# Kernel tuning notes

Hardware: AMD Instinct MI355X
Metric: run time of the kernel (lower is better)

## Reference

```python
import jax, jax.numpy as jnp
import numpy as np

N, E, Z, C, B, G, T = 10000, 160000, 10, 64, 8, 16, 2
R_MAX = 5.0
AVG_NEIGH = 16.0
L_SLICES = ((0, 1), (1, 4), (4, 9))  # l=0,1,2 blocks of the 9 SH components


def sph_harm(u):
    # component-normalized real spherical harmonics up to l=2, u: [E,3] unit vectors
    x, y, z = u[:, 0], u[:, 1], u[:, 2]
    s3, s5, s15 = 3.0 ** 0.5, 5.0 ** 0.5, 15.0 ** 0.5
    return jnp.stack([
        jnp.ones_like(x),
        s3 * x, s3 * y, s3 * z,
        s15 * x * y, s15 * y * z, (s5 / 2) * (3 * z * z - 1), s15 * x * z, (s15 / 2) * (x * x - y * y),
    ], axis=1)  # [E,9]


def radial_embed(r):
    # Bessel basis * polynomial cutoff (p=5), r: [E]
    u = r / R_MAX
    n = jnp.arange(1, B + 1, dtype=jnp.float32)
    bessel = jnp.sqrt(2.0 / R_MAX) * jnp.sin(n[None, :] * jnp.pi * u[:, None]) / (r[:, None] + 1e-9)
    p = 5.0
    fc = 1 - (p + 1) * (p + 2) / 2 * u ** p + p * (p + 2) * u ** (p + 1) - p * (p + 1) / 2 * u ** (p + 2)
    fc = jnp.where(u < 1.0, fc, 0.0)
    return bessel * fc[:, None]  # [E,B]


def per_l_linear(x, W):
    # x: [n,C,9], W: [3,C,C]; independent channel mixing per l-block
    return jnp.concatenate([
        jnp.einsum('ncm,cd->ndm', x[:, :, s:e], W[l]) for l, (s, e) in enumerate(L_SLICES)
    ], axis=2)


def _forward(positions, node_attrs, charges, shifts, W_emb, atomic_energies,
             W_r1, W_r2, W_mix, W_sc, w_poly, W_prod, w_e, w_d,
             edge_index, batch, num_graphs):
    sender, receiver = edge_index[0], edge_index[1]
    # atomic reference energies
    node_e0 = node_attrs @ atomic_energies  # [N]
    e0 = jax.ops.segment_sum(node_e0, batch, num_segments=num_graphs)
    # node embedding: scalars only
    node_feats = jnp.zeros((positions.shape[0], C, 9), positions.dtype)
    node_feats = node_feats.at[:, :, 0].set(node_attrs @ W_emb)
    # edge geometry
    vec = positions[sender] - positions[receiver] + shifts  # [E,3]
    lengths = jnp.sqrt(jnp.sum(vec * vec, axis=1) + 1e-12)
    sh = sph_harm(vec / lengths[:, None])        # [E,9]
    edge_feats = radial_embed(lengths)           # [E,B]
    energies = [e0]
    dipoles = []
    for t in range(T):
        # radial MLP -> per-channel TP weights
        w = jax.nn.silu(edge_feats @ W_r1[t]) @ W_r2[t]      # [E,C]
        h_s = node_feats[sender, :, 0]                       # gather sender scalars [E,C]
        m = (w * h_s)[:, :, None] * sh[:, None, :]           # TP message [E,C,9]
        agg = jax.ops.segment_sum(m, receiver, num_segments=positions.shape[0]) / AVG_NEIGH
        msg = per_l_linear(agg, W_mix[t])
        sc = per_l_linear(node_feats, W_sc[t])               # self-connection
        # product basis (correlation 3): channel-wise scalar polynomial gate
        s0 = msg[:, :, 0]
        poly = w_poly[t, :, 0][None] + w_poly[t, :, 1][None] * s0 + w_poly[t, :, 2][None] * s0 * s0
        node_feats = per_l_linear(msg * poly[:, :, None], W_prod[t]) + sc
        # readout: 1x0e energy + 1x1o dipole
        e_n = node_feats[:, :, 0] @ w_e[t]                   # [N]
        energies.append(jax.ops.segment_sum(e_n, batch, num_segments=num_graphs))
        dipoles.append(jnp.einsum('ncm,c->nm', node_feats[:, :, 1:4], w_d[t]))  # [N,3]
    contributions = jnp.stack(energies, axis=-1)             # [G,T+1]
    total_energy = jnp.sum(contributions, axis=-1)           # [G]
    atomic_dipoles = jnp.sum(jnp.stack(dipoles, axis=-1), axis=-1)  # [N,3]
    total_dipole = jax.ops.segment_sum(atomic_dipoles, batch, num_segments=num_graphs)
    total_dipole = total_dipole + jax.ops.segment_sum(charges[:, None] * positions, batch, num_segments=num_graphs)
    return total_energy, contributions, atomic_dipoles, total_dipole


def setup_inputs():
    key = jax.random.key(0)
    ks = jax.random.split(key, 16)
    s = 0.1
    species = jax.random.randint(ks[1], (N,), 0, Z)
    return {
        'positions': jax.random.normal(ks[0], (N, 3)) * 3.0,
        'node_attrs': jax.nn.one_hot(species, Z, dtype=jnp.float32),
        'charges': jax.random.normal(ks[2], (N,)) * 0.1,
        'shifts': jnp.zeros((E, 3), jnp.float32),
        'W_emb': jax.random.normal(ks[5], (Z, C)) * s,
        'atomic_energies': jax.random.normal(ks[6], (Z,)) * s,
        'W_r1': jax.random.normal(ks[7], (T, B, 64)) * s,
        'W_r2': jax.random.normal(ks[8], (T, 64, C)) * s,
        'W_mix': jax.random.normal(ks[9], (T, 3, C, C)) * s,
        'W_sc': jax.random.normal(ks[10], (T, 3, C, C)) * s,
        'w_poly': jax.random.normal(ks[11], (T, C, 3)) * s,
        'W_prod': jax.random.normal(ks[12], (T, 3, C, C)) * s,
        'w_e': jax.random.normal(ks[13], (T, C)) * s,
        'w_d': jax.random.normal(ks[14], (T, C)) * s,
        'edge_index': jax.random.randint(ks[3], (2, E), 0, N),
        'batch': jnp.sort(jax.random.randint(ks[4], (N,), 0, G)),
        'num_graphs': G,
    }


def reference(positions, node_attrs, charges, shifts, W_emb, atomic_energies,
              W_r1, W_r2, W_mix, W_sc, w_poly, W_prod, w_e, w_d,
              edge_index, batch, num_graphs):
    args = (node_attrs, charges, shifts, W_emb, atomic_energies, W_r1, W_r2,
            W_mix, W_sc, w_poly, W_prod, w_e, w_d, edge_index, batch, num_graphs)
    total_energy, contributions, atomic_dipoles, total_dipole = _forward(positions, *args)
    forces = -jax.grad(lambda p: jnp.sum(_forward(p, *args)[0]))(positions)
    return total_energy, contributions, forces, total_dipole, atomic_dipoles
```

## Files before the change

### kernel.cpp

```cpp
#include <hip/hip_runtime.h>
#include <hip/hip_bf16.h>

#define NN 10000
#define NE 160000
#define NZ 10
#define NBES 8
#define NG 16
#define NT 2
#define NB 2048
#define NB1 2049
#define PL ((size_t)NN*64)

static constexpr float PI_F  = 3.14159265358979323846f;
static constexpr float KBES  = 0.63245553203367587f;
static constexpr float S3    = 1.73205080756887729f;

static constexpr size_t OFF_UVL  = 0;
static constexpr size_t OFF_PIN  = OFF_UVL + (size_t)NE*4;
static constexpr size_t OFF_ATT  = OFF_PIN + (size_t)NN*3;
static constexpr size_t OFF_CHG  = OFF_ATT + (size_t)NN*NZ;
static constexpr size_t OFF_SHF  = OFF_CHG + (size_t)NN;
static constexpr size_t OFF_NF0  = OFF_SHF + (size_t)NE*3;
static constexpr size_t OFF_NF1  = OFF_NF0 + PL;
static constexpr size_t OFF_MSG0 = OFF_NF1 + 4*PL;
static constexpr size_t OFF_MSG1 = OFF_MSG0 + 4*PL;
static constexpr size_t OFF_AGG  = OFF_MSG1 + 4*PL;
static constexpr size_t O_GA1    = OFF_MSG0 + PL;
static constexpr size_t O_GA0    = OFF_AGG;
static constexpr size_t OFF_W    = OFF_AGG + 4*PL;
static constexpr size_t O_WEMB   = OFF_W;
static constexpr size_t O_AE     = O_WEMB + 640;
static constexpr size_t O_R1     = O_AE   + 16;
static constexpr size_t O_R2     = O_R1   + 1024;
static constexpr size_t O_WMIX   = O_R2   + 8192;
static constexpr size_t O_WMIXT  = O_WMIX + 24576;
static constexpr size_t O_WSC    = O_WMIXT+ 24576;
static constexpr size_t O_WSCT   = O_WSC  + 24576;
static constexpr size_t O_WPROD  = O_WSCT + 24576;
static constexpr size_t O_WPRODT = O_WPROD+ 24576;
static constexpr size_t O_WPOLY  = O_WPRODT+24576;
static constexpr size_t O_WE     = O_WPOLY+ 384;
static constexpr size_t O_WD     = O_WE   + 128;
static constexpr size_t OFF_ACC  = O_WD   + 128;
static constexpr size_t O_E0G    = OFF_ACC;
static constexpr size_t O_ETG    = O_E0G + 16;
static constexpr size_t O_TD     = O_ETG + 32;
static constexpr size_t O_ADP    = O_TD  + 48;
static constexpr size_t O_GPOS   = O_ADP + (size_t)NN*3;
static constexpr size_t ACC_FLOATS = 96 + (size_t)NN*6;
static constexpr size_t O_EN0    = O_GPOS + (size_t)NN*3;
static constexpr size_t O_EN1    = O_EN0 + NN;
static constexpr size_t O_E0N    = O_EN1 + NN;
static constexpr size_t O_FLAG   = O_E0N + NN;
static constexpr size_t O_TW     = O_FLAG + 4;
static constexpr size_t O_TQ     = O_TW + (size_t)2*NB1*128;
static constexpr size_t O_OFFR   = O_TQ + (size_t)2*NB1*128;
static constexpr size_t O_OFFS   = O_OFFR + (NN+1);
static constexpr size_t O_CURR   = O_OFFS + (NN+1);
static constexpr size_t O_CURS   = O_CURR + NN;
static constexpr size_t O_RECRAW = O_CURS + NN;
static constexpr size_t O_RECR   = (O_RECRAW + 7) & ~(size_t)7;
static constexpr size_t O_RECS   = O_RECR + (size_t)NE*8 + 64;
static constexpr size_t WS_FLOATS= O_RECS + (size_t)NE*8 + 64;

__device__ __forceinline__ float rlane(float v, int l){
  return __int_as_float(__builtin_amdgcn_readlane(__float_as_int(v), l));
}
__device__ __forceinline__ int irlane(float v, int l){
  return __builtin_amdgcn_readlane(__float_as_int(v), l);
}

static constexpr int LD_CNT[14] = {NN*3, NN*NZ, NN, NE*3, NZ*64, NZ, NT*NBES*64, NT*64*64,
                                   NT*3*64*64, NT*3*64*64, NT*64*3, NT*3*64*64, NT*64, NT*64};
static constexpr int LD_TOTAL = NN*3 + NN*NZ + NN + NE*3 + NZ*64 + NZ + NT*NBES*64 + NT*64*64
                              + 3*(NT*3*64*64) + NT*64*3 + 4*(NT*64) - NT*64*2;
__global__ __launch_bounds__(256) void k_load_all(
    const void* s0, const void* s1, const void* s2, const void* s3, const void* s4,
    const void* s5, const void* s6, const void* s7, const void* s8, const void* s9,
    const void* s10, const void* s11, const void* s12, const void* s13,
    float* __restrict__ ws){
  __shared__ int found;
  if (threadIdx.x == 0) found = 0;
  __syncthreads();
  const unsigned* raw = (const unsigned*)s1;
  int f = 0;
  for (int i = threadIdx.x; i < 4096; i += 256){
    unsigned w = raw[i];
    f |= (w == 0x00003F80u || w == 0x3F803F80u) ? 1 : 0;
  }
  if (f) found = 1;
  __syncthreads();
  const int isbf = found;
  if (blockIdx.x == 0 && threadIdx.x == 0) ((int*)(ws + O_FLAG))[0] = isbf;

  const void* srcs[14] = {s0,s1,s2,s3,s4,s5,s6,s7,s8,s9,s10,s11,s12,s13};
  const size_t dsts[14] = {OFF_PIN, OFF_ATT, OFF_CHG, OFF_SHF, O_WEMB, O_AE, O_R1, O_R2,
                           O_WMIX, O_WSC, O_WPOLY, O_WPROD, O_WE, O_WD};
  int i = blockIdx.x*256 + threadIdx.x;
  int seg = -1, off = i;
  #pragma unroll
  for (int j = 0; j < 14; ++j){
    if (seg < 0){
      if (off < LD_CNT[j]) seg = j;
      else off -= LD_CNT[j];
    }
  }
  if (seg < 0) return;
  float v = isbf ? __bfloat162float(((const __hip_bfloat16*)srcs[seg])[off])
                 : ((const float*)srcs[seg])[off];
  ws[dsts[seg] + off] = v;
}

static constexpr int GEOM_B = (NE+255)/256;
static constexpr int TAB_B  = (2*NB1+3)/4;
static constexpr int INIT_B = (NN+3)/4;
static constexpr int TRAN_B = 5*4096/256;
__global__ __launch_bounds__(256, 3) void k_prep(float* __restrict__ ws, const int* __restrict__ ei){
  int b = blockIdx.x;
  if (b < GEOM_B){
    int e = b*256 + threadIdx.x;
    if (e >= NE) return;
    const float* pos = ws + OFF_PIN;
    const float* shifts = ws + OFF_SHF;
    int s = ei[e], r = ei[NE + e];
    float vx = pos[s*3+0] - pos[r*3+0] + shifts[(size_t)e*3+0];
    float vy = pos[s*3+1] - pos[r*3+1] + shifts[(size_t)e*3+1];
    float vz = pos[s*3+2] - pos[r*3+2] + shifts[(size_t)e*3+2];
    float L = sqrtf(vx*vx + vy*vy + vz*vz + 1e-12f);
    float inv = 1.f / L;
    float4 uq; uq.x = vx*inv; uq.y = vy*inv; uq.z = vz*inv; uq.w = L;
    *(float4*)(ws + OFF_UVL + (size_t)e*4) = uq;
    if (L < 5.f){
      atomicAdd((int*)(ws + O_CURR) + r, 1);
      atomicAdd((int*)(ws + O_CURS) + s, 1);
    }
  } else if (b < GEOM_B + TAB_B){
    int lane = threadIdx.x & 63;
    int task = (b - GEOM_B)*4 + (threadIdx.x >> 6);
    if (task >= 2*NB1) return;
    int t = task / NB1, node = task % NB1;
    const float* R1 = ws + O_R1 + (size_t)t*512;
    const float* R2 = ws + O_R2 + (size_t)t*4096;
    float r1c[8];
    #pragma unroll
    for (int j = 0; j < 8; ++j) r1c[j] = R1[j*64 + lane];
    float L = fmaxf((float)node * (5.f/NB), 1e-6f);
    float ur = L*0.2f;
    float ef[8], dd[8];
    if (ur < 1.f){
      float u2=ur*ur, u4=u2*u2, u5=u4*ur;
      float fc = 1.f - 21.f*u5 + 35.f*u5*ur - 15.f*u5*u2;
      float omu = 1.f - ur;
      float dfc = -105.f*u4*omu*omu;
      float invr = 1.f/(L + 1e-9f);
      #pragma unroll
      for (int bb = 0; bb < 8; ++bb){
        float nb = (float)(bb+1);
        float arg = nb*PI_F*ur;
        float sn = __sinf(arg), cs = __cosf(arg);
        float bes = KBES*sn*invr;
        float dbes = KBES*(nb*PI_F*0.2f)*cs*invr - bes*invr;
        ef[bb] = bes*fc;
        dd[bb] = dbes*fc + bes*dfc*0.2f;
      }
    } else {
      #pragma unroll
      for (int bb = 0; bb < 8; ++bb){ ef[bb] = 0.f; dd[bb] = 0.f; }
    }
    float a = 0.f, tt = 0.f;
    #pragma unroll
    for (int bb = 0; bb < 8; ++bb){ a = fmaf(ef[bb], r1c[bb], a); tt = fmaf(r1c[bb], dd[bb], tt); }
    float sg = 1.f/(1.f + __expf(-a));
    float sl = a*sg;
    float q  = sg*fmaf(a, 1.f - sg, 1.f)*tt;
    float r2c[64];
    #pragma unroll
    for (int j = 0; j < 64; ++j) r2c[j] = R2[j*64 + lane];
    float W0=0.f, W1=0.f, Q0=0.f, Q1=0.f;
    #pragma unroll
    for (int j = 0; j < 64; j += 2){
      W0 = fmaf(rlane(sl, j  ), r2c[j  ], W0);
      W1 = fmaf(rlane(sl, j+1), r2c[j+1], W1);
      Q0 = fmaf(rlane(q,  j  ), r2c[j  ], Q0);
      Q1 = fmaf(rlane(q,  j+1), r2c[j+1], Q1);
    }
    float Wv = (W0+W1)*(1.f/16.f);
    float Qv = (Q0+Q1)*(1.f/16.f);
    size_t base2 = ((size_t)t*NB1 + node)*128 + (size_t)lane*2;
    ws[O_TW + base2] = Wv;
    ws[O_TQ + base2] = Qv;
    if (node > 0){
      ws[O_TW + base2 - 128 + 1] = Wv;
      ws[O_TQ + base2 - 128 + 1] = Qv;
    }
  } else if (b < GEOM_B + TAB_B + INIT_B){
    int lane = threadIdx.x & 63;
    int n = (b - GEOM_B - TAB_B)*4 + (threadIdx.x >> 6);
    if (n >= NN) return;
    const float* attrs = ws + OFF_ATT;
    float acc = 0.f;
    #pragma unroll
    for (int z = 0; z < NZ; ++z) acc = fmaf(attrs[(size_t)n*NZ+z], ws[O_WEMB + z*64 + lane], acc);
    ws[OFF_NF0 + (size_t)n*64 + lane] = acc;
    if (lane == 0){
      float e = 0.f;
      #pragma unroll
      for (int z = 0; z < NZ; ++z) e = fmaf(attrs[(size_t)n*NZ+z], ws[O_AE + z], e);
      ws[O_E0N + n] = e;
    }
  } else {
    int i = (b - GEOM_B - TAB_B - INIT_B)*256 + threadIdx.x;
    int mat = i >> 12, r = (i >> 6) & 63, c = i & 63;
    const size_t src[5] = {O_WMIX, O_WMIX+12288, O_WPROD, O_WPROD+12288, O_WSC+12288};
    const size_t dst[5] = {O_WMIXT, O_WMIXT+12288, O_WPRODT, O_WPRODT+12288, O_WSCT+12288};
    ws[dst[mat] + (size_t)c*64 + r] = ws[src[mat] + (size_t)r*64 + c];
  }
}

__global__ __launch_bounds__(1024) void k_csr_scan(
    int* __restrict__ curr, int* __restrict__ curs,
    int* __restrict__ offr, int* __restrict__ offs_){
  __shared__ unsigned short cr[NN], cs[NN];
  __shared__ int pr[1024], ps[1024];
  int tid = threadIdx.x;
  for (int i = tid; i < NN; i += 1024){
    cr[i] = (unsigned short)curr[i];
    cs[i] = (unsigned short)curs[i];
  }
  __syncthreads();
  const int chunk = (NN + 1023)/1024;
  int lo = tid*chunk, hi = lo + chunk;
  if (hi > NN) hi = NN;
  if (lo > NN) lo = NN;
  int sr = 0, ss = 0;
  for (int i = lo; i < hi; ++i){ sr += cr[i]; ss += cs[i]; }
  pr[tid] = sr; ps[tid] = ss;
  __syncthreads();
  for (int o = 1; o < 1024; o <<= 1){
    int vr = (tid >= o) ? pr[tid-o] : 0;
    int vs = (tid >= o) ? ps[tid-o] : 0;
    __syncthreads();
    pr[tid] += vr; ps[tid] += vs;
    __syncthreads();
  }
  int runr = tid ? pr[tid-1] : 0;
  int runs = tid ? ps[tid-1] : 0;
  for (int i = lo; i < hi; ++i){
    int a = cr[i], c = cs[i];
    offr[i] = runr; curr[i] = runr; runr += a;
    offs_[i] = runs; curs[i] = runs; runs += c;
  }
  if (tid == 1023){ offr[NN] = runr; offs_[NN] = runs; }
}

__global__ void k_csr_fill(const int* __restrict__ ei, const float* __restrict__ uvl,
                           int* __restrict__ curr, int* __restrict__ curs,
                           float* __restrict__ recr, float* __restrict__ recs){
  int e = blockIdx.x*256 + threadIdx.x;
  if (e >= NE) return;
  float4 q = *(const float4*)(uvl + (size_t)e*4);
  if (q.w >= 5.f) return;
  int s = ei[e], r = ei[NE + e];
  int4 meta; meta.x = s; meta.y = r; meta.z = e; meta.w = 0;
  int pr = atomicAdd(&curr[r], 1);
  *(float4*)(recr + (size_t)pr*8) = q;
  *(int4*)(recr + (size_t)pr*8 + 4) = meta;
  int ps = atomicAdd(&curs[s], 1);
  *(float4*)(recs + (size_t)ps*8) = q;
  *(int4*)(recs + (size_t)ps*8 + 4) = meta;
}

__global__ __launch_bounds__(256, 4) void k_agg(
    const float* __restrict__ TWt, const float* __restrict__ recr,
    const float* __restrict__ h, const int* __restrict__ offr,
    float* __restrict__ agg){
  int lane = threadIdx.x & 63;
  int wid = blockIdx.x*4 + (threadIdx.x >> 6);
  int nw  = gridDim.x*4;
  for (int n = wid; n < NN; n += nw){
    int lo = offr[n], hi = offr[n+1];
    float c0=0.f, x1=0.f, y1=0.f, z1=0.f;
    if (lo < hi){
      float rv = recr[(size_t)lo*8 + lane];
      for (int i = lo; i < hi; ){
        int ni = i + 8;
        float rvn = (ni < hi) ? recr[(size_t)ni*8 + lane] : 0.f;
        int cnt = hi - i;
        if (cnt >= 8){
          #pragma unroll
          for (int j = 0; j < 8; ++j){
            float ux = rlane(rv, j*8+0), uy = rlane(rv, j*8+1), uz = rlane(rv, j*8+2);
            float L  = rlane(rv, j*8+3);
            int   s  = irlane(rv, j*8+4);
            float pos = L*(NB/5.f); int bi = (int)pos; float f = pos - (float)bi;
            const float2 tp = *(const float2*)(TWt + ((size_t)bi*64 + lane)*2);
            float w = fmaf(tp.y - tp.x, f, tp.x);
            float wh = w * h[(size_t)s*64 + lane];
            c0 += wh;
            x1 = fmaf(wh, ux, x1);
            y1 = fmaf(wh, uy, y1);
            z1 = fmaf(wh, uz, z1);
          }
        } else {
          for (int j = 0; j < cnt; ++j){
            float ux = rlane(rv, j*8+0), uy = rlane(rv, j*8+1), uz = rlane(rv, j*8+2);
            float L  = rlane(rv, j*8+3);
            int   s  = irlane(rv, j*8+4);
            float pos = L*(NB/5.f); int bi = (int)pos; float f = pos - (float)bi;
            const float2 tp = *(const float2*)(TWt + ((size_t)bi*64 + lane)*2);
            float w = fmaf(tp.y - tp.x, f, tp.x);
            float wh = w * h[(size_t)s*64 + lane];
            c0 += wh;
            x1 = fmaf(wh, ux, x1);
            y1 = fmaf(wh, uy, y1);
            z1 = fmaf(wh, uz, z1);
          }
        }
        rv = rvn; i = ni;
      }
    }
    size_t ob = (size_t)n*64 + lane;
    agg[ob]        = c0;
    agg[ob+PL]     = S3*x1;
    agg[ob+2*PL]   = S3*y1;
    agg[ob+3*PL]   = S3*z1;
  }
}

template<int GB1>
__global__ __launch_bounds__(256, 3) void k_lin2(
    const float* __restrict__ in, const float* __restrict__ W3, float* __restrict__ out,
    const float* __restrict__ WMIXT1, const float* __restrict__ WPRODT1,
    const float* __restrict__ we1, const float* __restrict__ wp1,
    float* __restrict__ ga1){
  int k = blockIdx.y;
  int l = (k==0) ? 0 : 1;
  const float* W = W3 + (size_t)l*4096;
  int lane = threadIdx.x & 63;
  float wcol[64];
  #pragma unroll
  for (int j = 0; j < 64; ++j) wcol[j] = W[j*64 + lane];
  float wcol2[64];
  float g = 0.f, p0 = 0.f, p1 = 0.f, p2 = 0.f;
  const bool gb1 = GB1 && (k == 0);
  if (gb1){
    #pragma unroll
    for (int j = 0; j < 64; ++j) wcol2[j] = WMIXT1[j*64 + lane];
    #pragma unroll
    for (int c = 0; c < 64; ++c) g = fmaf(we1[c], WPRODT1[c*64 + lane], g);
    p0 = wp1[lane*3]; p1 = wp1[lane*3+1]; p2 = wp1[lane*3+2];
  }
  int wid = blockIdx.x*4 + (threadIdx.x >> 6);
  int nw  = gridDim.x*4;
  const float* inp = in + (size_t)k*PL;
  float* outp = out + (size_t)k*PL;
  for (int n = wid; n < NN; n += nw){
    float x = inp[(size_t)n*64 + lane];
    float a0 = 0.f, a1 = 0.f, a2 = 0.f, a3 = 0.f;
    #pragma unroll
    for (int j = 0; j < 64; j += 4){
      a0 = fmaf(rlane(x, j  ), wcol[j  ], a0);
      a1 = fmaf(rlane(x, j+1), wcol[j+1], a1);
      a2 = fmaf(rlane(x, j+2), wcol[j+2], a2);
      a3 = fmaf(rlane(x, j+3), wcol[j+3], a3);
    }
    float m = (a0+a1) + (a2+a3);
    outp[(size_t)n*64 + lane] = m;
    if (gb1){
      float poly = fmaf(fmaf(p2, m, p1), m, p0);
      float dp   = fmaf(2.f*p2, m, p1);
      float gb = g*fmaf(m, dp, poly);
      float b0=0.f, b1=0.f, b2=0.f, b3=0.f;
      #pragma unroll
      for (int j = 0; j < 64; j += 4){
        b0 = fmaf(rlane(gb, j  ), wcol2[j  ], b0);
        b1 = fmaf(rlane(gb, j+1), wcol2[j+1], b1);
        b2 = fmaf(rlane(gb, j+2), wcol2[j+2], b2);
        b3 = fmaf(rlane(gb, j+3), wcol2[j+3], b3);
      }
      ga1[(size_t)n*64 + lane] = (b0+b1) + (b2+b3);
    }
  }
}

template<int WRITE_NF, int NF_SINGLE>
__global__ __launch_bounds__(256, 3) void k_tail(
    const float* __restrict__ nf_in, const float* __restrict__ msg,
    const float* __restrict__ Wsc, const float* __restrict__ Wprod, const float* __restrict__ wp,
    const float* __restrict__ we, const float* __restrict__ wd,
    float* __restrict__ nf_out, float* __restrict__ en, float* __restrict__ adp){
  int lane = threadIdx.x & 63;
  int k = threadIdx.x >> 6;
  int l = (k==0) ? 0 : 1;
  const bool use_sc = !(NF_SINGLE && k > 0);
  float wcs[64], wcp[64];
  #pragma unroll
  for (int j = 0; j < 64; ++j)
    wcp[j] = Wprod[(size_t)l*4096 + j*64 + lane];
  if (use_sc){
    #pragma unroll
    for (int j = 0; j < 64; ++j)
      wcs[j] = Wsc[(size_t)l*4096 + j*64 + lane];
  }
  float p0 = wp[lane*3], p1 = wp[lane*3+1], p2 = wp[lane*3+2];
  float rw = (k==0) ? we[lane] : wd[lane];
  const float* msgk = msg + (size_t)k*PL;
  const float* nfk  = nf_in + (size_t)k*PL;
  float* outk = nf_out + (size_t)k*PL;
  for (int n = blockIdx.x; n < NN; n += gridDim.x){
    size_t base = (size_t)n*64 + lane;
    float s0 = msg[base];
    float xm = (k==0) ? s0 : msgk[base];
    float xg = xm * fmaf(fmaf(p2, s0, p1), s0, p0);
    float b0=0.f, b1=0.f;
    #pragma unroll
    for (int j = 0; j < 64; j += 2){
      b0 = fmaf(rlane(xg, j  ), wcp[j  ], b0);
      b1 = fmaf(rlane(xg, j+1), wcp[j+1], b1);
    }
    float out = b0 + b1;
    if (use_sc){
      float xs = nfk[base];
      float a0=0.f, a1=0.f;
      #pragma unroll
      for (int j = 0; j < 64; j += 2){
        a0 = fmaf(rlane(xs, j  ), wcs[j  ], a0);
        a1 = fmaf(rlane(xs, j+1), wcs[j+1], a1);
      }
      out += a0 + a1;
    }
    if (WRITE_NF) outk[base] = out;
    float red = out * rw;
    #pragma unroll
    for (int o = 32; o; o >>= 1) red += __shfl_xor(red, o, 64);
    if (lane == 0){
      if (k == 0) en[n] = red;
      else        adp[n*3 + (k-1)] += red;
    }
  }
}

static constexpr int GHG_GRID = 1024;
static constexpr int RED_B = (NN+255)/256;
__global__ __launch_bounds__(256, 2) void k_ghg0(float* __restrict__ ws, const int* __restrict__ offs_,
                                                 const int* __restrict__ batch){
  if (blockIdx.x >= GHG_GRID){
    int n = (blockIdx.x - GHG_GRID)*256 + threadIdx.x;
    int lane = threadIdx.x & 63;
    bool valid = (n < NN);
    int g = valid ? batch[n] : -1;
    float v0=0.f, v1=0.f, v2=0.f, tx=0.f, ty=0.f, tz=0.f;
    if (valid){
      v0 = ws[O_E0N + n]; v1 = ws[O_EN0 + n]; v2 = ws[O_EN1 + n];
      float qq = ws[OFF_CHG + n];
      tx = ws[O_ADP + n*3+0] + qq*ws[OFF_PIN + n*3+0];
      ty = ws[O_ADP + n*3+1] + qq*ws[OFF_PIN + n*3+1];
      tz = ws[O_ADP + n*3+2] + qq*ws[OFF_PIN + n*3+2];
    }
    float* e0g = ws + O_E0G; float* Etg = ws + O_ETG; float* td = ws + O_TD;
    int g0 = __shfl(g, 0, 64), g63 = __shfl(g, 63, 64);
    if (g0 == g63 && g0 >= 0){
      #pragma unroll
      for (int o = 32; o; o >>= 1){
        v0 += __shfl_xor(v0, o, 64); v1 += __shfl_xor(v1, o, 64); v2 += __shfl_xor(v2, o, 64);
        tx += __shfl_xor(tx, o, 64); ty += __shfl_xor(ty, o, 64); tz += __shfl_xor(tz, o, 64);
      }
      if (lane == 0){
        atomicAdd(&e0g[g0], v0); atomicAdd(&Etg[g0], v1); atomicAdd(&Etg[16+g0], v2);
        atomicAdd(&td[g0*3+0], tx); atomicAdd(&td[g0*3+1], ty); atomicAdd(&td[g0*3+2], tz);
      }
    } else if (valid){
      atomicAdd(&e0g[g], v0); atomicAdd(&Etg[g], v1); atomicAdd(&Etg[16+g], v2);
      atomicAdd(&td[g*3+0], tx); atomicAdd(&td[g*3+1], ty); atomicAdd(&td[g*3+2], tz);
    }
    return;
  }
  const int lane = threadIdx.x & 63;
  float wcp[64], wcm[64];
  #pragma unroll
  for (int j = 0; j < 64; ++j) wcp[j] = ws[O_WPRODT + j*64 + lane];
  #pragma unroll
  for (int j = 0; j < 64; ++j) wcm[j] = ws[O_WMIXT + j*64 + lane];
  int wid = blockIdx.x*4 + (threadIdx.x >> 6);
  const int nw = GHG_GRID*4;
  float gnfc = ws[O_WE + lane];
  {
    const float* WS1 = ws + O_WSCT + 12288;
    const float* we1 = ws + O_WE + 64;
    #pragma unroll
    for (int c = 0; c < 64; ++c) gnfc = fmaf(we1[c], WS1[c*64 + lane], gnfc);
  }
  const float p0 = ws[O_WPOLY + lane*3];
  const float p1 = ws[O_WPOLY + lane*3 + 1];
  const float p2 = ws[O_WPOLY + lane*3 + 2];
  const float* TW1 = ws + O_TW + (size_t)NB1*128;
  const float* recs = ws + O_RECS;
  const float* GA1 = ws + O_GA1;
  for (int n = wid; n < NN; n += nw){
    int lo = offs_[n], hi = offs_[n+1];
    float acc = 0.f;
    if (lo < hi){
      float rv = recs[(size_t)lo*8 + lane];
      for (int i = lo; i < hi; ){
        int ni = i + 8;
        float rvn = (ni < hi) ? recs[(size_t)ni*8 + lane] : 0.f;
        int cnt = hi - i;
        if (cnt >= 8){
          #pragma unroll
          for (int j = 0; j < 8; ++j){
            float L = rlane(rv, j*8+3);
            int   r = irlane(rv, j*8+5);
            float pos = L*(NB/5.f); int bi = (int)pos; float f = pos - (float)bi;
            const float2 tp = *(const float2*)(TW1 + ((size_t)bi*64 + lane)*2);
            float w = fmaf(tp.y - tp.x, f, tp.x);
            acc = fmaf(w, GA1[(size_t)r*64 + lane], acc);
          }
        } else {
          for (int j = 0; j < cnt; ++j){
            float L = rlane(rv, j*8+3);
            int   r = irlane(rv, j*8+5);
            float pos = L*(NB/5.f); int bi = (int)pos; float f = pos - (float)bi;
            const float2 tp = *(const float2*)(TW1 + ((size_t)bi*64 + lane)*2);
            float w = fmaf(tp.y - tp.x, f, tp.x);
            acc = fmaf(w, GA1[(size_t)r*64 + lane], acc);
          }
        }
        rv = rvn; i = ni;
      }
    }
    float gB = gnfc + acc;
    float q0=0.f, q1=0.f;
    #pragma unroll
    for (int j = 0; j < 64; j += 2){
      q0 = fmaf(rlane(gB,j),   wcp[j  ], q0);
      q1 = fmaf(rlane(gB,j+1), wcp[j+1], q1);
    }
    float gmp = q0 + q1;
    float s0v = ws[OFF_MSG0 + (size_t)n*64 + lane];
    float poly = fmaf(fmaf(p2, s0v, p1), s0v, p0);
    float dp   = fmaf(2.f*p2, s0v, p1);
    float gb = gmp * fmaf(s0v, dp, poly);
    float u0=0.f, u1=0.f;
    #pragma unroll
    for (int j = 0; j < 64; j += 2){
      u0 = fmaf(rlane(gb,j),   wcm[j  ], u0);
      u1 = fmaf(rlane(gb,j+1), wcm[j+1], u1);
    }
    ws[O_GA0 + (size_t)n*64 + lane] = u0 + u1;
  }
}

__global__ __launch_bounds__(256, 4) void k_bwdE2(float* __restrict__ ws, const int* __restrict__ nlive_ptr){
  const int lane = threadIdx.x & 63;
  int wid = blockIdx.x*4 + (threadIdx.x >> 6);
  const int nw = gridDim.x*4;
  const int nlive = nlive_ptr[0];
  const int ngrp = (nlive + 7) >> 3;
  const float* recs = ws + O_RECS;
  const float* TQ0 = ws + O_TQ;
  const float* TQ1 = ws + O_TQ + (size_t)NB1*128;
  const float* h0  = ws + OFF_NF0;
  const float* h1  = ws + OFF_NF1;
  const float* ga0 = ws + O_GA0;
  const float* ga1 = ws + O_GA1;
  float* gpos = ws + O_GPOS;
  for (int gi = wid; gi < ngrp; gi += nw){
    const int i0 = gi*8;
    float rv = recs[(size_t)i0*8 + lane];
    int cnt = nlive - i0; if (cnt > 8) cnt = 8;
    #pragma unroll 8
    for (int j = 0; j < cnt; ++j){
      float ux = rlane(rv, j*8+0), uy = rlane(rv, j*8+1), uz = rlane(rv, j*8+2);
      float L  = rlane(rv, j*8+3);
      int   s  = irlane(rv, j*8+4);
      int   r  = irlane(rv, j*8+5);
      float pos = L*(NB/5.f); int bi = (int)pos; float f = pos - (float)bi;
      const float2 t0 = *(const float2*)(TQ0 + ((size_t)bi*64 + lane)*2);
      const float2 t1 = *(const float2*)(TQ1 + ((size_t)bi*64 + lane)*2);
      float Q0 = fmaf(t0.y - t0.x, f, t0.x);
      float Q1 = fmaf(t1.y - t1.x, f, t1.x);
      float rr = Q0*h0[(size_t)s*64 + lane]*ga0[(size_t)r*64 + lane]
               + Q1*h1[(size_t)s*64 + lane]*ga1[(size_t)r*64 + lane];
      #pragma unroll
      for (int o = 32; o; o >>= 1) rr += __shfl_xor(rr, o, 64);
      if (lane < 3){
        float u = (lane==0) ? ux : ((lane==1) ? uy : uz);
        float v = rr*u;
        atomicAdd(&gpos[(size_t)s*3 + lane],  v);
        atomicAdd(&gpos[(size_t)r*3 + lane], -v);
      }
    }
  }
}

__global__ void k_writeout(const float* __restrict__ e0g, const float* __restrict__ Etg,
                           const float* __restrict__ td, const float* __restrict__ adp,
                           const float* __restrict__ gpos, void* __restrict__ outv,
                           const int* __restrict__ flag){
  int i = blockIdx.x*256 + threadIdx.x;
  const int total = NG + NG*3 + NN*3 + NG*3 + NN*3;
  if (i >= total) return;
  float v;
  if (i < 16){
    v = e0g[i] + Etg[i] + Etg[16+i];
  } else if (i < 64){
    int j = i - 16; int g = j/3, t = j - g*3;
    v = (t == 0) ? e0g[g] : Etg[(t-1)*16 + g];
  } else if (i < 64 + NN*3){
    v = -gpos[i-64];
  } else if (i < 64 + NN*3 + 48){
    v = td[i - (64 + NN*3)];
  } else {
    v = adp[i - (64 + NN*3 + 48)];
  }
  if (flag[0]) ((__hip_bfloat16*)outv)[i] = __float2bfloat16(v);
  else         ((float*)outv)[i] = v;
}

extern "C" void kernel_launch(void* const* d_in, const int* in_sizes, int n_in,
                              void* d_out, int out_size, void* d_ws, size_t ws_size,
                              hipStream_t stream) {
  if (ws_size < WS_FLOATS*sizeof(float)) return;
  const int* ei    = (const int*)d_in[14];
  const int* batch = (const int*)d_in[15];
  float* ws = (float*)d_ws;

  int* offr  = (int*)(ws + O_OFFR);
  int* offs_ = (int*)(ws + O_OFFS);
  int* curr  = (int*)(ws + O_CURR);
  int* curs  = (int*)(ws + O_CURS);

  hipMemsetAsync(ws + OFF_ACC, 0, ACC_FLOATS*sizeof(float), stream);
  hipMemsetAsync(curr, 0, 2*NN*sizeof(int), stream);

  k_load_all<<<(LD_TOTAL+255)/256, 256, 0, stream>>>(
      d_in[0], d_in[1], d_in[2], d_in[3], d_in[4], d_in[5], d_in[6], d_in[7],
      d_in[8], d_in[9], d_in[10], d_in[11], d_in[12], d_in[13], ws);
  k_prep<<<GEOM_B + TAB_B + INIT_B + TRAN_B, 256, 0, stream>>>(ws, ei);
  k_csr_scan<<<1, 1024, 0, stream>>>(curr, curs, offr, offs_);
  k_csr_fill<<<(NE+255)/256, 256, 0, stream>>>(ei, ws+OFF_UVL, curr, curs,
                                               ws+O_RECR, ws+O_RECS);

  dim3 ling(256, 4);

  k_agg<<<1024, 256, 0, stream>>>(ws+O_TW, ws+O_RECR, ws+OFF_NF0, offr, ws+OFF_AGG);
  k_lin2<0><<<ling, 256, 0, stream>>>(ws+OFF_AGG, ws+O_WMIX, ws+OFF_MSG0,
                                      ws, ws, ws, ws, ws);
  k_tail<1,1><<<1024, 256, 0, stream>>>(ws+OFF_NF0, ws+OFF_MSG0,
                                        ws+O_WSC, ws+O_WPROD,
                                        ws+O_WPOLY, ws+O_WE, ws+O_WD,
                                        ws+OFF_NF1, ws+O_EN0, ws+O_ADP);
  k_agg<<<1024, 256, 0, stream>>>(ws+O_TW + (size_t)NB1*128, ws+O_RECR, ws+OFF_NF1, offr, ws+OFF_AGG);
  k_lin2<1><<<ling, 256, 0, stream>>>(ws+OFF_AGG, ws+O_WMIX + 12288, ws+OFF_MSG1,
                                      ws+O_WMIXT + 12288, ws+O_WPRODT + 12288,
                                      ws+O_WE + 64, ws+O_WPOLY + 192, ws+O_GA1);
  k_tail<0,0><<<1024, 256, 0, stream>>>(ws+OFF_NF1, ws+OFF_MSG1,
                                        ws+O_WSC + 12288, ws+O_WPROD + 12288,
                                        ws+O_WPOLY + 192, ws+O_WE + 64, ws+O_WD + 64,
                                        ws+OFF_NF1, ws+O_EN1, ws+O_ADP);

  k_ghg0<<<GHG_GRID + RED_B, 256, 0, stream>>>(ws, offs_, batch);
  k_bwdE2<<<2048, 256, 0, stream>>>(ws, offs_ + NN);

  k_writeout<<<(60112+255)/256, 256, 0, stream>>>(ws+O_E0G, ws+O_ETG, ws+O_TD, ws+O_ADP,
                                                  ws+O_GPOS, d_out, (const int*)(ws+O_FLAG));
}
```

Before: 335.0 us.

## Replace CSR construction with compacted edge list and atomic scatter aggregation

After: 387.7 us. 1.16x slower.

```diff
diff --git a/kernel.cpp b/kernel.cpp
--- a/kernel.cpp
+++ b/kernel.cpp
@@ -27,6 +27,7 @@
 static constexpr size_t OFF_AGG  = OFF_MSG1 + 4*PL;
 static constexpr size_t O_GA1    = OFF_MSG0 + PL;
 static constexpr size_t O_GA0    = OFF_AGG;
+static constexpr size_t O_GB0    = OFF_AGG + PL;
 static constexpr size_t OFF_W    = OFF_AGG + 4*PL;
 static constexpr size_t O_WEMB   = OFF_W;
 static constexpr size_t O_AE     = O_WEMB + 640;
@@ -54,13 +55,8 @@
 static constexpr size_t O_FLAG   = O_E0N + NN;
 static constexpr size_t O_TW     = O_FLAG + 4;
 static constexpr size_t O_TQ     = O_TW + (size_t)2*NB1*128;
-static constexpr size_t O_OFFR   = O_TQ + (size_t)2*NB1*128;
-static constexpr size_t O_OFFS   = O_OFFR + (NN+1);
-static constexpr size_t O_CURR   = O_OFFS + (NN+1);
-static constexpr size_t O_CURS   = O_CURR + NN;
-static constexpr size_t O_RECRAW = O_CURS + NN;
-static constexpr size_t O_RECR   = (O_RECRAW + 7) & ~(size_t)7;
-static constexpr size_t O_RECS   = O_RECR + (size_t)NE*8 + 64;
+static constexpr size_t O_RECRAW = O_TQ + (size_t)2*NB1*128;
+static constexpr size_t O_RECS   = (O_RECRAW + 7) & ~(size_t)7;
 static constexpr size_t WS_FLOATS= O_RECS + (size_t)NE*8 + 64;
 
 __device__ __forceinline__ float rlane(float v, int l){
@@ -127,12 +123,14 @@
     float vy = pos[s*3+1] - pos[r*3+1] + shifts[(size_t)e*3+1];
     float vz = pos[s*3+2] - pos[r*3+2] + shifts[(size_t)e*3+2];
     float L = sqrtf(vx*vx + vy*vy + vz*vz + 1e-12f);
-    float inv = 1.f / L;
-    float4 uq; uq.x = vx*inv; uq.y = vy*inv; uq.z = vz*inv; uq.w = L;
-    *(float4*)(ws + OFF_UVL + (size_t)e*4) = uq;
     if (L < 5.f){
-      atomicAdd((int*)(ws + O_CURR) + r, 1);
-      atomicAdd((int*)(ws + O_CURS) + s, 1);
+      int p = atomicAdd((int*)(ws + O_FLAG) + 1, 1);
+      float inv = 1.f / L;
+      float* rec = ws + O_RECS + (size_t)p*8;
+      float4 uq; uq.x = vx*inv; uq.y = vy*inv; uq.z = vz*inv; uq.w = L;
+      *(float4*)rec = uq;
+      int4 meta; meta.x = s; meta.y = r; meta.z = e; meta.w = 0;
+      *(int4*)(rec + 4) = meta;
     }
   } else if (b < GEOM_B + TAB_B){
     int lane = threadIdx.x & 63;
@@ -217,119 +215,41 @@
   }
 }
 
-__global__ __launch_bounds__(1024) void k_csr_scan(
-    int* __restrict__ curr, int* __restrict__ curs,
-    int* __restrict__ offr, int* __restrict__ offs_){
-  __shared__ unsigned short cr[NN], cs[NN];
-  __shared__ int pr[1024], ps[1024];
-  int tid = threadIdx.x;
-  for (int i = tid; i < NN; i += 1024){
-    cr[i] = (unsigned short)curr[i];
-    cs[i] = (unsigned short)curs[i];
-  }
-  __syncthreads();
-  const int chunk = (NN + 1023)/1024;
-  int lo = tid*chunk, hi = lo + chunk;
-  if (hi > NN) hi = NN;
-  if (lo > NN) lo = NN;
-  int sr = 0, ss = 0;
-  for (int i = lo; i < hi; ++i){ sr += cr[i]; ss += cs[i]; }
-  pr[tid] = sr; ps[tid] = ss;
-  __syncthreads();
-  for (int o = 1; o < 1024; o <<= 1){
-    int vr = (tid >= o) ? pr[tid-o] : 0;
-    int vs = (tid >= o) ? ps[tid-o] : 0;
-    __syncthreads();
-    pr[tid] += vr; ps[tid] += vs;
-    __syncthreads();
-  }
-  int runr = tid ? pr[tid-1] : 0;
-  int runs = tid ? ps[tid-1] : 0;
-  for (int i = lo; i < hi; ++i){
-    int a = cr[i], c = cs[i];
-    offr[i] = runr; curr[i] = runr; runr += a;
-    offs_[i] = runs; curs[i] = runs; runs += c;
-  }
-  if (tid == 1023){ offr[NN] = runr; offs_[NN] = runs; }
-}
-
-__global__ void k_csr_fill(const int* __restrict__ ei, const float* __restrict__ uvl,
-                           int* __restrict__ curr, int* __restrict__ curs,
-                           float* __restrict__ recr, float* __restrict__ recs){
-  int e = blockIdx.x*256 + threadIdx.x;
-  if (e >= NE) return;
-  float4 q = *(const float4*)(uvl + (size_t)e*4);
-  if (q.w >= 5.f) return;
-  int s = ei[e], r = ei[NE + e];
-  int4 meta; meta.x = s; meta.y = r; meta.z = e; meta.w = 0;
-  int pr = atomicAdd(&curr[r], 1);
-  *(float4*)(recr + (size_t)pr*8) = q;
-  *(int4*)(recr + (size_t)pr*8 + 4) = meta;
-  int ps = atomicAdd(&curs[s], 1);
-  *(float4*)(recs + (size_t)ps*8) = q;
-  *(int4*)(recs + (size_t)ps*8 + 4) = meta;
-}
-
-__global__ __launch_bounds__(256, 4) void k_agg(
-    const float* __restrict__ TWt, const float* __restrict__ recr,
-    const float* __restrict__ h, const int* __restrict__ offr,
+__global__ __launch_bounds__(256, 4) void k_aggE(
+    const float* __restrict__ TWt, const float* __restrict__ recs,
+    const int* __restrict__ nlive_ptr, const float* __restrict__ h,
     float* __restrict__ agg){
-  int lane = threadIdx.x & 63;
+  const int lane = threadIdx.x & 63;
   int wid = blockIdx.x*4 + (threadIdx.x >> 6);
-  int nw  = gridDim.x*4;
-  for (int n = wid; n < NN; n += nw){
-    int lo = offr[n], hi = offr[n+1];
-    float c0=0.f, x1=0.f, y1=0.f, z1=0.f;
-    if (lo < hi){
-      float rv = recr[(size_t)lo*8 + lane];
-      for (int i = lo; i < hi; ){
-        int ni = i + 8;
-        float rvn = (ni < hi) ? recr[(size_t)ni*8 + lane] : 0.f;
-        int cnt = hi - i;
-        if (cnt >= 8){
-          #pragma unroll
-          for (int j = 0; j < 8; ++j){
-            float ux = rlane(rv, j*8+0), uy = rlane(rv, j*8+1), uz = rlane(rv, j*8+2);
-            float L  = rlane(rv, j*8+3);
-            int   s  = irlane(rv, j*8+4);
-            float pos = L*(NB/5.f); int bi = (int)pos; float f = pos - (float)bi;
-            const float2 tp = *(const float2*)(TWt + ((size_t)bi*64 + lane)*2);
-            float w = fmaf(tp.y - tp.x, f, tp.x);
-            float wh = w * h[(size_t)s*64 + lane];
-            c0 += wh;
-            x1 = fmaf(wh, ux, x1);
-            y1 = fmaf(wh, uy, y1);
-            z1 = fmaf(wh, uz, z1);
-          }
-        } else {
-          for (int j = 0; j < cnt; ++j){
-            float ux = rlane(rv, j*8+0), uy = rlane(rv, j*8+1), uz = rlane(rv, j*8+2);
-            float L  = rlane(rv, j*8+3);
-            int   s  = irlane(rv, j*8+4);
-            float pos = L*(NB/5.f); int bi = (int)pos; float f = pos - (float)bi;
-            const float2 tp = *(const float2*)(TWt + ((size_t)bi*64 + lane)*2);
-            float w = fmaf(tp.y - tp.x, f, tp.x);
-            float wh = w * h[(size_t)s*64 + lane];
-            c0 += wh;
-            x1 = fmaf(wh, ux, x1);
-            y1 = fmaf(wh, uy, y1);
-            z1 = fmaf(wh, uz, z1);
-          }
-        }
-        rv = rvn; i = ni;
-      }
-    }
-    size_t ob = (size_t)n*64 + lane;
-    agg[ob]        = c0;
-    agg[ob+PL]     = S3*x1;
-    agg[ob+2*PL]   = S3*y1;
-    agg[ob+3*PL]   = S3*z1;
+  const int nw = gridDim.x*4;
+  const int nlive = nlive_ptr[0];
+  const int ngrp = (nlive + 7) >> 3;
+  for (int gi = wid; gi < ngrp; gi += nw){
+    const int i0 = gi*8;
+    float rv = recs[(size_t)i0*8 + lane];
+    int cnt = nlive - i0; if (cnt > 8) cnt = 8;
+    #pragma unroll 8
+    for (int j = 0; j < cnt; ++j){
+      float ux = rlane(rv, j*8+0), uy = rlane(rv, j*8+1), uz = rlane(rv, j*8+2);
+      float L  = rlane(rv, j*8+3);
+      int   s  = irlane(rv, j*8+4);
+      int   r  = irlane(rv, j*8+5);
+      float pos = L*(NB/5.f); int bi = (int)pos; float f = pos - (float)bi;
+      const float2 tp = *(const float2*)(TWt + ((size_t)bi*64 + lane)*2);
+      float w = fmaf(tp.y - tp.x, f, tp.x);
+      float wh = w * h[(size_t)s*64 + lane];
+      size_t ob = (size_t)r*64 + lane;
+      atomicAdd(&agg[ob],        wh);
+      atomicAdd(&agg[ob + PL],   wh*(S3*ux));
+      atomicAdd(&agg[ob + 2*PL], wh*(S3*uy));
+      atomicAdd(&agg[ob + 3*PL], wh*(S3*uz));
+    }
   }
 }
 
 template<int GB1>
 __global__ __launch_bounds__(256, 3) void k_lin2(
-    const float* __restrict__ in, const float* __restrict__ W3, float* __restrict__ out,
+    float* __restrict__ in, const float* __restrict__ W3, float* __restrict__ out,
     const float* __restrict__ WMIXT1, const float* __restrict__ WPRODT1,
     const float* __restrict__ we1, const float* __restrict__ wp1,
     float* __restrict__ ga1){
@@ -352,10 +272,12 @@
   }
   int wid = blockIdx.x*4 + (threadIdx.x >> 6);
   int nw  = gridDim.x*4;
-  const float* inp = in + (size_t)k*PL;
+  float* inp = in + (size_t)k*PL;
   float* outp = out + (size_t)k*PL;
   for (int n = wid; n < NN; n += nw){
-    float x = inp[(size_t)n*64 + lane];
+    size_t idx = (size_t)n*64 + lane;
+    float x = inp[idx];
+    inp[idx] = 0.f;
     float a0 = 0.f, a1 = 0.f, a2 = 0.f, a3 = 0.f;
     #pragma unroll
     for (int j = 0; j < 64; j += 4){
@@ -365,7 +287,7 @@
       a3 = fmaf(rlane(x, j+3), wcol[j+3], a3);
     }
     float m = (a0+a1) + (a2+a3);
-    outp[(size_t)n*64 + lane] = m;
+    outp[idx] = m;
     if (gb1){
       float poly = fmaf(fmaf(p2, m, p1), m, p0);
       float dp   = fmaf(2.f*p2, m, p1);
@@ -378,7 +300,7 @@
         b2 = fmaf(rlane(gb, j+2), wcol2[j+2], b2);
         b3 = fmaf(rlane(gb, j+3), wcol2[j+3], b3);
       }
-      ga1[(size_t)n*64 + lane] = (b0+b1) + (b2+b3);
+      ga1[idx] = (b0+b1) + (b2+b3);
     }
   }
 }
@@ -440,12 +362,38 @@
   }
 }
 
-static constexpr int GHG_GRID = 1024;
+__global__ __launch_bounds__(256, 4) void k_ghgE(float* __restrict__ ws, const int* __restrict__ nlive_ptr){
+  const int lane = threadIdx.x & 63;
+  int wid = blockIdx.x*4 + (threadIdx.x >> 6);
+  const int nw = gridDim.x*4;
+  const int nlive = nlive_ptr[0];
+  const int ngrp = (nlive + 7) >> 3;
+  const float* recs = ws + O_RECS;
+  const float* TW1 = ws + O_TW + (size_t)NB1*128;
+  const float* GA1 = ws + O_GA1;
+  float* gb0 = ws + O_GB0;
+  for (int gi = wid; gi < ngrp; gi += nw){
+    const int i0 = gi*8;
+    float rv = recs[(size_t)i0*8 + lane];
+    int cnt = nlive - i0; if (cnt > 8) cnt = 8;
+    #pragma unroll 8
+    for (int j = 0; j < cnt; ++j){
+      float L = rlane(rv, j*8+3);
+      int   s = irlane(rv, j*8+4);
+      int   r = irlane(rv, j*8+5);
+      float pos = L*(NB/5.f); int bi = (int)pos; float f = pos - (float)bi;
+      const float2 tp = *(const float2*)(TW1 + ((size_t)bi*64 + lane)*2);
+      float w = fmaf(tp.y - tp.x, f, tp.x);
+      atomicAdd(&gb0[(size_t)s*64 + lane], w * GA1[(size_t)r*64 + lane]);
+    }
+  }
+}
+
+static constexpr int GB_GRID = 1024;
 static constexpr int RED_B = (NN+255)/256;
-__global__ __launch_bounds__(256, 2) void k_ghg0(float* __restrict__ ws, const int* __restrict__ offs_,
-                                                 const int* __restrict__ batch){
-  if (blockIdx.x >= GHG_GRID){
-    int n = (blockIdx.x - GHG_GRID)*256 + threadIdx.x;
+__global__ __launch_bounds__(256, 3) void k_gb0(float* __restrict__ ws, const int* __restrict__ batch){
+  if (blockIdx.x >= GB_GRID){
+    int n = (blockIdx.x - GB_GRID)*256 + threadIdx.x;
     int lane = threadIdx.x & 63;
     bool valid = (n < NN);
     int g = valid ? batch[n] : -1;
@@ -481,8 +429,6 @@
   for (int j = 0; j < 64; ++j) wcp[j] = ws[O_WPRODT + j*64 + lane];
   #pragma unroll
   for (int j = 0; j < 64; ++j) wcm[j] = ws[O_WMIXT + j*64 + lane];
-  int wid = blockIdx.x*4 + (threadIdx.x >> 6);
-  const int nw = GHG_GRID*4;
   float gnfc = ws[O_WE + lane];
   {
     const float* WS1 = ws + O_WSCT + 12288;
@@ -493,42 +439,12 @@
   const float p0 = ws[O_WPOLY + lane*3];
   const float p1 = ws[O_WPOLY + lane*3 + 1];
   const float p2 = ws[O_WPOLY + lane*3 + 2];
-  const float* TW1 = ws + O_TW + (size_t)NB1*128;
-  const float* recs = ws + O_RECS;
-  const float* GA1 = ws + O_GA1;
+  const float* gb0 = ws + O_GB0;
+  int wid = blockIdx.x*4 + (threadIdx.x >> 6);
+  const int nw = GB_GRID*4;
   for (int n = wid; n < NN; n += nw){
-    int lo = offs_[n], hi = offs_[n+1];
-    float acc = 0.f;
-    if (lo < hi){
-      float rv = recs[(size_t)lo*8 + lane];
-      for (int i = lo; i < hi; ){
-        int ni = i + 8;
-        float rvn = (ni < hi) ? recs[(size_t)ni*8 + lane] : 0.f;
-        int cnt = hi - i;
-        if (cnt >= 8){
-          #pragma unroll
-          for (int j = 0; j < 8; ++j){
-            float L = rlane(rv, j*8+3);
-            int   r = irlane(rv, j*8+5);
-            float pos = L*(NB/5.f); int bi = (int)pos; float f = pos - (float)bi;
-            const float2 tp = *(const float2*)(TW1 + ((size_t)bi*64 + lane)*2);
-            float w = fmaf(tp.y - tp.x, f, tp.x);
-            acc = fmaf(w, GA1[(size_t)r*64 + lane], acc);
-          }
-        } else {
-          for (int j = 0; j < cnt; ++j){
-            float L = rlane(rv, j*8+3);
-            int   r = irlane(rv, j*8+5);
-            float pos = L*(NB/5.f); int bi = (int)pos; float f = pos - (float)bi;
-            const float2 tp = *(const float2*)(TW1 + ((size_t)bi*64 + lane)*2);
-            float w = fmaf(tp.y - tp.x, f, tp.x);
-            acc = fmaf(w, GA1[(size_t)r*64 + lane], acc);
-          }
-        }
-        rv = rvn; i = ni;
-      }
-    }
-    float gB = gnfc + acc;
+    size_t idx = (size_t)n*64 + lane;
+    float gB = gnfc + gb0[idx];
     float q0=0.f, q1=0.f;
     #pragma unroll
     for (int j = 0; j < 64; j += 2){
@@ -536,7 +452,7 @@
       q1 = fmaf(rlane(gB,j+1), wcp[j+1], q1);
     }
     float gmp = q0 + q1;
-    float s0v = ws[OFF_MSG0 + (size_t)n*64 + lane];
+    float s0v = ws[OFF_MSG0 + idx];
     float poly = fmaf(fmaf(p2, s0v, p1), s0v, p0);
     float dp   = fmaf(2.f*p2, s0v, p1);
     float gb = gmp * fmaf(s0v, dp, poly);
@@ -546,7 +462,7 @@
       u0 = fmaf(rlane(gb,j),   wcm[j  ], u0);
       u1 = fmaf(rlane(gb,j+1), wcm[j+1], u1);
     }
-    ws[O_GA0 + (size_t)n*64 + lane] = u0 + u1;
+    ws[O_GA0 + idx] = u0 + u1;
   }
 }
 
@@ -624,33 +540,27 @@
   const int* ei    = (const int*)d_in[14];
   const int* batch = (const int*)d_in[15];
   float* ws = (float*)d_ws;
-
-  int* offr  = (int*)(ws + O_OFFR);
-  int* offs_ = (int*)(ws + O_OFFS);
-  int* curr  = (int*)(ws + O_CURR);
-  int* curs  = (int*)(ws + O_CURS);
+  int* nl = (int*)(ws + O_FLAG) + 1;
 
   hipMemsetAsync(ws + OFF_ACC, 0, ACC_FLOATS*sizeof(float), stream);
-  hipMemsetAsync(curr, 0, 2*NN*sizeof(int), stream);
+  hipMemsetAsync(ws + OFF_AGG, 0, 4*PL*sizeof(float), stream);
+  hipMemsetAsync(nl, 0, sizeof(int), stream);
 
   k_load_all<<<(LD_TOTAL+255)/256, 256, 0, stream>>>(
       d_in[0], d_in[1], d_in[2], d_in[3], d_in[4], d_in[5], d_in[6], d_in[7],
       d_in[8], d_in[9], d_in[10], d_in[11], d_in[12], d_in[13], ws);
   k_prep<<<GEOM_B + TAB_B + INIT_B + TRAN_B, 256, 0, stream>>>(ws, ei);
-  k_csr_scan<<<1, 1024, 0, stream>>>(curr, curs, offr, offs_);
-  k_csr_fill<<<(NE+255)/256, 256, 0, stream>>>(ei, ws+OFF_UVL, curr, curs,
-                                               ws+O_RECR, ws+O_RECS);
 
   dim3 ling(256, 4);
 
-  k_agg<<<1024, 256, 0, stream>>>(ws+O_TW, ws+O_RECR, ws+OFF_NF0, offr, ws+OFF_AGG);
+  k_aggE<<<2048, 256, 0, stream>>>(ws+O_TW, ws+O_RECS, nl, ws+OFF_NF0, ws+OFF_AGG);
   k_lin2<0><<<ling, 256, 0, stream>>>(ws+OFF_AGG, ws+O_WMIX, ws+OFF_MSG0,
                                       ws, ws, ws, ws, ws);
   k_tail<1,1><<<1024, 256, 0, stream>>>(ws+OFF_NF0, ws+OFF_MSG0,
                                         ws+O_WSC, ws+O_WPROD,
                                         ws+O_WPOLY, ws+O_WE, ws+O_WD,
                                         ws+OFF_NF1, ws+O_EN0, ws+O_ADP);
-  k_agg<<<1024, 256, 0, stream>>>(ws+O_TW + (size_t)NB1*128, ws+O_RECR, ws+OFF_NF1, offr, ws+OFF_AGG);
+  k_aggE<<<2048, 256, 0, stream>>>(ws+O_TW + (size_t)NB1*128, ws+O_RECS, nl, ws+OFF_NF1, ws+OFF_AGG);
   k_lin2<1><<<ling, 256, 0, stream>>>(ws+OFF_AGG, ws+O_WMIX + 12288, ws+OFF_MSG1,
                                       ws+O_WMIXT + 12288, ws+O_WPRODT + 12288,
                                       ws+O_WE + 64, ws+O_WPOLY + 192, ws+O_GA1);
@@ -659,8 +569,9 @@
                                         ws+O_WPOLY + 192, ws+O_WE + 64, ws+O_WD + 64,
                                         ws+OFF_NF1, ws+O_EN1, ws+O_ADP);
 
-  k_ghg0<<<GHG_GRID + RED_B, 256, 0, stream>>>(ws, offs_, batch);
-  k_bwdE2<<<2048, 256, 0, stream>>>(ws, offs_ + NN);
+  k_ghgE<<<2048, 256, 0, stream>>>(ws, nl);
+  k_gb0<<<GB_GRID + RED_B, 256, 0, stream>>>(ws, batch);
+  k_bwdE2<<<2048, 256, 0, stream>>>(ws, nl);
 
   k_writeout<<<(60112+255)/256, 256, 0, stream>>>(ws+O_E0G, ws+O_ETG, ws+O_TD, ws+O_ADP,
                                                   ws+O_GPOS, d_out, (const int*)(ws+O_FLAG));
```
